# Performance work log

Hardware: AMD Instinct MI355X
Metric: run time of the kernel (lower is better)

## Reference

```python
import jax, jax.numpy as jnp
import numpy as np

B, S, D, H = 2, 2048, 1024, 16
DH = D // H
SCALE = 1.0 / float(np.sqrt(DH))


def setup_inputs() -> dict:
    key = jax.random.key(0)
    ks = jax.random.split(key, 9)
    std = 1.0 / float(np.sqrt(D))
    x = jax.random.normal(ks[0], (B, S, D), dtype=jnp.float32)
    # causal mask: True = masked (future positions)
    mask = jnp.triu(jnp.ones((S, S), dtype=bool), k=1)
    Wq = jax.random.normal(ks[1], (D, D), dtype=jnp.float32) * std
    Wk = jax.random.normal(ks[2], (D, D), dtype=jnp.float32) * std
    Wv = jax.random.normal(ks[3], (D, D), dtype=jnp.float32) * std
    Wo = jax.random.normal(ks[4], (D, D), dtype=jnp.float32) * std
    bq = jax.random.normal(ks[5], (D,), dtype=jnp.float32) * 0.01
    bk = jax.random.normal(ks[6], (D,), dtype=jnp.float32) * 0.01
    bv = jax.random.normal(ks[7], (D,), dtype=jnp.float32) * 0.01
    bo = jax.random.normal(ks[8], (D,), dtype=jnp.float32) * 0.01
    return {"x": x, "mask": mask, "Wq": Wq, "bq": bq, "Wk": Wk, "bk": bk,
            "Wv": Wv, "bv": bv, "Wo": Wo, "bo": bo}


def _split_heads(t):
    # (B, S, D) -> (B, H, S, DH)
    return t.reshape(B, S, H, DH).transpose(0, 2, 1, 3)


def reference(x, mask, Wq, bq, Wk, bk, Wv, bv, Wo, bo):
    # torch nn.Linear: y = x @ W.T + b
    q = _split_heads(x @ Wq.T + bq)
    k = _split_heads(x @ Wk.T + bk)
    v = _split_heads(x @ Wv.T + bv)
    # scores: (B, H, S, S)
    scores = jnp.einsum('bhsd,bhtd->bhst', q, k) * SCALE
    scores = jnp.where(mask[None, None, :, :], jnp.float32(-1e9), scores)
    attn = jax.nn.softmax(scores, axis=-1)
    attn = jnp.nan_to_num(attn, nan=0.0)
    out = jnp.einsum('bhst,bhtd->bhsd', attn, v)
    out = out.transpose(0, 2, 1, 3).reshape(B, S, D)
    return out @ Wo.T + bo
```

## Files before the change

### kernel.cpp

```cpp
#include <hip/hip_runtime.h>

#define S_LEN  2048
#define DMODEL 1024
#define NHEAD  16
#define DHEAD  64
#define SCALE_F 0.125f
#define SL2E_F 0.180336880f

typedef unsigned short ushort_t;
typedef __attribute__((ext_vector_type(8))) short bf16x8;
typedef __attribute__((ext_vector_type(4))) float f32x4;

typedef __attribute__((address_space(1))) void gv_t;
typedef __attribute__((address_space(3))) void lv_t;

__device__ __forceinline__ ushort_t f2bf(float f) {
    unsigned u = __builtin_bit_cast(unsigned, f);
    unsigned r = (u + 0x7FFFu + ((u >> 16) & 1u)) >> 16;
    return (ushort_t)r;
}

__device__ __forceinline__ unsigned cvtpk_bf16(float a, float b) {
    unsigned r;
    asm("v_cvt_pk_bf16_f32 %0, %1, %2" : "=v"(r) : "v"(a), "v"(b));
    return r;
}

__device__ __forceinline__ void gload16(const ushort_t* g, ushort_t* l) {
    __builtin_amdgcn_global_load_lds((gv_t*)g, (lv_t*)l, 16, 0, 0);
}

template<int N> __device__ __forceinline__ void wait_vmcnt() {
    if constexpr (N == 8)      asm volatile("s_waitcnt vmcnt(8)" ::: "memory");
    else if constexpr (N == 6) asm volatile("s_waitcnt vmcnt(6)" ::: "memory");
    else if constexpr (N == 4) asm volatile("s_waitcnt vmcnt(4)" ::: "memory");
    else if constexpr (N == 3) asm volatile("s_waitcnt vmcnt(3)" ::: "memory");
    else                       asm volatile("s_waitcnt vmcnt(0)" ::: "memory");
}

__global__ void cast_all(const float* __restrict__ x,
                         const float* __restrict__ Wq, const float* __restrict__ Wk,
                         const float* __restrict__ Wv, const float* __restrict__ Wo,
                         ushort_t* __restrict__ dst, int n4) {
    int i = blockIdx.x * blockDim.x + threadIdx.x;
    int stride = gridDim.x * blockDim.x;
    for (int idx = i; idx < n4; idx += stride) {
        const float* src; int off;
        if (idx < 1048576)      { src = x;  off = idx; }
        else if (idx < 1310720) { src = Wq; off = idx - 1048576; }
        else if (idx < 1572864) { src = Wk; off = idx - 1310720; }
        else if (idx < 1835008) { src = Wv; off = idx - 1572864; }
        else                    { src = Wo; off = idx - 1835008; }
        float4 f = ((const float4*)src)[off];
        ushort4 o;
        o.x = f2bf(f.x); o.y = f2bf(f.y); o.z = f2bf(f.z); o.w = f2bf(f.w);
        ((ushort4*)dst)[idx] = o;
    }
}

template<int MODE, int BM>
__launch_bounds__(256)
__global__ void gemm_bt(const ushort_t* __restrict__ A, const ushort_t* __restrict__ Bw,
                        const float* __restrict__ b0, const float* __restrict__ b1,
                        const float* __restrict__ b2,
                        void* __restrict__ out0, void* __restrict__ out1, void* __restrict__ out2,
                        int M, int N, int K) {
    constexpr int MF = BM / 32;
    constexpr int NLOADS = BM / 64 + 2;
    __shared__ ushort_t As[2][BM][32];
    __shared__ ushort_t Bs[2][128][32];
    const int tid  = threadIdx.x;
    const int lane = tid & 63;
    const int w    = tid >> 6;
    const int wr   = w >> 1, wc = w & 1;
    const int m0   = blockIdx.x * BM;
    const int n0   = blockIdx.y * 128;
    const int l15  = lane & 15;
    const int lg   = lane >> 4;
    const int srow = lane >> 2;
    const int scol = ((lane & 3) ^ ((lane >> 3) & 3)) * 8;
    const int ck   = (l15 >> 1) & 3;

    f32x4 acc[MF][4] = {};

    auto stage = [&](int buf, int k0) {
#pragma unroll
        for (int j = 0; j < BM / 64; j++) {
            const int rg = (w * (BM / 64) + j) * 16;
            gload16(A + (size_t)(m0 + rg + srow) * K + k0 + scol, &As[buf][rg][0]);
        }
#pragma unroll
        for (int j = 0; j < 2; j++) {
            const int rg = (w * 2 + j) * 16;
            gload16(Bw + (size_t)(n0 + rg + srow) * K + k0 + scol, &Bs[buf][rg][0]);
        }
    };

    stage(0, 0);
    int buf = 0;

    for (int k0 = 0; k0 < K; k0 += 32) {
        if (k0 + 32 < K) {
            stage(buf ^ 1, k0 + 32);
            wait_vmcnt<NLOADS>();
        } else {
            wait_vmcnt<0>();
        }
        __builtin_amdgcn_s_barrier();
        __builtin_amdgcn_sched_barrier(0);

        bf16x8 af[MF], bfr[4];
#pragma unroll
        for (int i = 0; i < MF; i++)
            af[i]  = *(const bf16x8*)&As[buf][wr*(BM/2) + i*16 + l15][(lg ^ ck) * 8];
#pragma unroll
        for (int i = 0; i < 4;  i++)
            bfr[i] = *(const bf16x8*)&Bs[buf][wc*64 + i*16 + l15][(lg ^ ck) * 8];

        __builtin_amdgcn_s_setprio(1);
#pragma unroll
        for (int mf = 0; mf < MF; mf++)
#pragma unroll
            for (int nf = 0; nf < 4; nf++)
                acc[mf][nf] = __builtin_amdgcn_mfma_f32_16x16x32_bf16(af[mf], bfr[nf], acc[mf][nf], 0, 0, 0);
        __builtin_amdgcn_s_setprio(0);

        asm volatile("s_waitcnt lgkmcnt(0)" ::: "memory");
        __builtin_amdgcn_sched_barrier(0);
        __builtin_amdgcn_s_barrier();
        buf ^= 1;
    }

#pragma unroll
    for (int mf = 0; mf < MF; mf++) {
#pragma unroll
        for (int nf = 0; nf < 4; nf++) {
            const int col = n0 + wc*64 + nf*16 + l15;
            if constexpr (MODE == 2) {
                const float bv = b0[col];
#pragma unroll
                for (int r = 0; r < 4; r++) {
                    const int row = m0 + wr*(BM/2) + mf*16 + lg*4 + r;
                    ((float*)out0)[(size_t)row * N + col] = acc[mf][nf][r] + bv;
                }
            } else {
                const int mat = col >> 10;
                const int c   = col & 1023;
                const int h   = c >> 6, dh = c & 63;
                const float* bp = (mat == 0) ? b0 : ((mat == 1) ? b1 : b2);
                const float bv = bp[c];
#pragma unroll
                for (int r = 0; r < 4; r++) {
                    const int row = m0 + wr*(BM/2) + mf*16 + lg*4 + r;
                    const int b = row >> 11, s = row & 2047;
                    float v = acc[mf][nf][r] + bv;
                    if (mat == 0) {
                        v *= SL2E_F;
                        ((ushort_t*)out0)[((size_t)(b*NHEAD + h) * S_LEN + s) * DHEAD + dh] = f2bf(v);
                    } else if (mat == 1)
                        ((ushort_t*)out1)[((size_t)(b*NHEAD + h) * S_LEN + s) * DHEAD + dh] = f2bf(v);
                    else
                        ((ushort_t*)out2)[((size_t)(b*NHEAD + h) * DHEAD + dh) * S_LEN + s] = f2bf(v);
                }
            }
        }
    }
}

__launch_bounds__(256, 4)
__global__ void attn_fwd(const ushort_t* __restrict__ Q, const ushort_t* __restrict__ Kh,
                         const ushort_t* __restrict__ Vt, ushort_t* __restrict__ Aout) {
    __shared__ ushort_t Ks[2][64][64];
    __shared__ ushort_t Vs[2][64][64];
    __shared__ ushort_t Ps[4][16][64];
    const int tid  = threadIdx.x;
    const int lane = tid & 63;
    const int w    = tid >> 6;
    const int l15  = lane & 15, lg = lane >> 4;
    const int bh   = blockIdx.x;
    const int y    = blockIdx.y;
    const int kq   = y >> 3, g0 = y & 7;
    const int qt   = (kq == 0) ? 2*g0 : (kq == 1) ? (31 - 2*g0)
                   : (kq == 2) ? (2*g0 + 1) : (30 - 2*g0);

    const size_t qkbase = (size_t)bh * S_LEN * DHEAD;
    const size_t vtbase = (size_t)bh * DHEAD * S_LEN;

    const int rsub  = lane >> 3;
    const int csw   = ((lane & 7) ^ rsub) * 8;
    const int swz   = (l15 & 7) * 8;
    const int psxor = (l15 & 7) << 4;

    const int qw = qt * 64 + w * 16;

    bf16x8 aq[2];
#pragma unroll
    for (int kc = 0; kc < 2; kc++)
        aq[kc] = *(const bf16x8*)(Q + qkbase + (size_t)(qw + l15) * DHEAD + kc*32 + lg*8);

    float m = -3.0e38f, l = 0.0f;
    f32x4 o[4] = {};

    auto stage = [&](int buf, int t) {
        const int kv0 = t * 64;
        const ushort_t* kp = Kh + qkbase + (size_t)kv0 * DHEAD;
        const ushort_t* vp = Vt + vtbase + kv0;
#pragma unroll
        for (int j2 = 0; j2 < 2; j2++) {
            const int j  = w * 2 + j2;
            const int rg = j * 8 + rsub;
            gload16(kp + (size_t)rg * DHEAD + csw, &Ks[buf][j*8][0]);
            gload16(vp + (size_t)rg * S_LEN + csw, &Vs[buf][j*8][0]);
        }
    };

    ushort_t* psw = &Ps[w][0][0];
    char* psrow = (char*)(psw + l15 * 64);

    stage(0, 0);
    int buf = 0;

    for (int t = 0; t <= qt; t++) {
        if (t < qt) {
            stage(buf ^ 1, t + 1);
            wait_vmcnt<4>();
        } else {
            wait_vmcnt<0>();
        }
        __builtin_amdgcn_s_barrier();
        __builtin_amdgcn_sched_barrier(0);

        f32x4 sacc[4] = {};
        __builtin_amdgcn_s_setprio(1);
#pragma unroll
        for (int kc = 0; kc < 2; kc++)
#pragma unroll
            for (int nf = 0; nf < 4; nf++) {
                bf16x8 bk = *(const bf16x8*)&Ks[buf][nf*16 + l15][(kc*32 + lg*8) ^ swz];
                sacc[nf] = __builtin_amdgcn_mfma_f32_16x16x32_bf16(bk, aq[kc], sacc[nf], 0, 0, 0);
            }
        __builtin_amdgcn_s_setprio(0);

        if (t == qt) {
            const int rowq = qw + l15;
            const int kv0  = t * 64;
#pragma unroll
            for (int nf = 0; nf < 4; nf++)
#pragma unroll
                for (int r = 0; r < 4; r++) {
                    const int colk = kv0 + nf*16 + lg*4 + r;
                    if (colk > rowq) sacc[nf][r] = -3.0e38f;
                }
        }

        float mnf[4];
#pragma unroll
        for (int nf = 0; nf < 4; nf++)
            mnf[nf] = fmaxf(fmaxf(sacc[nf][0], sacc[nf][1]), fmaxf(sacc[nf][2], sacc[nf][3]));
        float mx = fmaxf(fmaxf(mnf[0], mnf[1]), fmaxf(mnf[2], mnf[3]));
        mx = fmaxf(mx, __shfl_xor(mx, 16));
        mx = fmaxf(mx, __shfl_xor(mx, 32));

        const bool skip = __all(mx <= m + 8.0f);
        const float mn = skip ? m : fmaxf(m, mx);

        float snf[4];
#pragma unroll
        for (int nf = 0; nf < 4; nf++) {
            const float p0 = exp2f(sacc[nf][0] - mn);
            const float p1 = exp2f(sacc[nf][1] - mn);
            const float p2 = exp2f(sacc[nf][2] - mn);
            const float p3 = exp2f(sacc[nf][3] - mn);
            uint2 pk;
            pk.x = cvtpk_bf16(p0, p1);
            pk.y = cvtpk_bf16(p2, p3);
            *(uint2*)(psrow + (((nf*16 + lg*4) * 2) ^ psxor)) = pk;
            snf[nf] = (p0 + p1) + (p2 + p3);
        }
        float s = (snf[0] + snf[1]) + (snf[2] + snf[3]);
        s += __shfl_xor(s, 16);
        s += __shfl_xor(s, 32);

        if (skip) {
            l += s;
        } else {
            const float corr = exp2f(m - mn);
            m = mn;
            l = l * corr + s;
            float cf[4];
#pragma unroll
            for (int r = 0; r < 4; r++) cf[r] = __shfl(corr, lg*4 + r);
#pragma unroll
            for (int nf = 0; nf < 4; nf++)
#pragma unroll
                for (int r = 0; r < 4; r++) o[nf][r] *= cf[r];
        }

        __builtin_amdgcn_s_setprio(1);
#pragma unroll
        for (int kc = 0; kc < 2; kc++) {
            bf16x8 pa = *(const bf16x8*)(psrow + (((kc*32 + lg*8) * 2) ^ psxor));
#pragma unroll
            for (int nf = 0; nf < 4; nf++) {
                bf16x8 bv = *(const bf16x8*)&Vs[buf][nf*16 + l15][(kc*32 + lg*8) ^ swz];
                o[nf] = __builtin_amdgcn_mfma_f32_16x16x32_bf16(pa, bv, o[nf], 0, 0, 0);
            }
        }
        __builtin_amdgcn_s_setprio(0);

        asm volatile("s_waitcnt lgkmcnt(0)" ::: "memory");
        __builtin_amdgcn_sched_barrier(0);
        __builtin_amdgcn_s_barrier();
        buf ^= 1;
    }

    const int b = bh >> 4, h = bh & 15;
    const float inv = 1.0f / l;
#pragma unroll
    for (int r = 0; r < 4; r++) {
        const float ia = __shfl(inv, lg*4 + r);
        const int rowq = qw + lg*4 + r;
#pragma unroll
        for (int nf = 0; nf < 4; nf++)
            Aout[((size_t)(b * S_LEN) + rowq) * DMODEL + h*DHEAD + nf*16 + l15] = f2bf(o[nf][r] * ia);
    }
}

extern "C" void kernel_launch(void* const* d_in, const int* in_sizes, int n_in,
                              void* d_out, int out_size, void* d_ws, size_t ws_size,
                              hipStream_t stream) {
    (void)in_sizes; (void)n_in; (void)out_size; (void)ws_size;
    const float* x  = (const float*)d_in[0];
    const float* Wq = (const float*)d_in[2];
    const float* bq = (const float*)d_in[3];
    const float* Wk = (const float*)d_in[4];
    const float* bk = (const float*)d_in[5];
    const float* Wv = (const float*)d_in[6];
    const float* bv = (const float*)d_in[7];
    const float* Wo = (const float*)d_in[8];
    const float* bo = (const float*)d_in[9];

    char* ws = (char*)d_ws;
    ushort_t* xb    = (ushort_t*)(ws);
    ushort_t* Wqkvb = (ushort_t*)(ws + (8u  << 20));
    ushort_t* Wob   = (ushort_t*)(ws + (14u << 20));
    ushort_t* Qh    = (ushort_t*)(ws + (16u << 20));
    ushort_t* Kh    = (ushort_t*)(ws + (24u << 20));
    ushort_t* Vth   = (ushort_t*)(ws + (32u << 20));
    ushort_t* Ao    = (ushort_t*)(ws + (40u << 20));

    cast_all<<<2048, 256, 0, stream>>>(x, Wq, Wk, Wv, Wo, xb, 2097152);

    gemm_bt<0, 128><<<dim3(32, 24), 256, 0, stream>>>(xb, Wqkvb, bq, bk, bv,
                                                      Qh, Kh, Vth, 2*S_LEN, 3*DMODEL, DMODEL);

    attn_fwd<<<dim3(2*NHEAD, 32), 256, 0, stream>>>(Qh, Kh, Vth, Ao);

    gemm_bt<2, 64><<<dim3(64, 8), 256, 0, stream>>>(Ao, Wob, bo, nullptr, nullptr,
                                                    d_out, nullptr, nullptr, 2*S_LEN, DMODEL, DMODEL);
}
```

Before: 115.5 us.

## Triple-buffer GEMM LDS staging, remap workgroups by XCD, drop trailing barriers

The GEMM kernel moves from double to triple-buffered LDS, prefetching two K-tiles ahead so each iteration needs one barrier instead of two. Workgroup IDs are remapped so consecutive tiles land on the same XCD (8-way interleave), which is meant to improve L2 reuse. The attention kernel now issues its next-tile prefetch after the barrier, waits for all loads, and drops the trailing barrier. The costs are more LDS per block, possibly lower occupancy, and in attention a full vmcnt wait that exposes load latency.

```diff
diff --git a/kernel.cpp b/kernel.cpp
--- a/kernel.cpp
+++ b/kernel.cpp
@@ -67,14 +67,21 @@
                         int M, int N, int K) {
     constexpr int MF = BM / 32;
     constexpr int NLOADS = BM / 64 + 2;
-    __shared__ ushort_t As[2][BM][32];
-    __shared__ ushort_t Bs[2][128][32];
+    __shared__ ushort_t As[3][BM][32];
+    __shared__ ushort_t Bs[3][128][32];
     const int tid  = threadIdx.x;
     const int lane = tid & 63;
     const int w    = tid >> 6;
     const int wr   = w >> 1, wc = w & 1;
-    const int m0   = blockIdx.x * BM;
-    const int n0   = blockIdx.y * 128;
+
+    const int gx  = gridDim.x;
+    const int nwg = gx * gridDim.y;
+    const int wg  = blockIdx.y * gx + blockIdx.x;
+    const int q8  = nwg >> 3;
+    const int nid = (wg & 7) * q8 + (wg >> 3);
+    const int m0  = (nid % gx) * BM;
+    const int n0  = (nid / gx) * 128;
+
     const int l15  = lane & 15;
     const int lg   = lane >> 4;
     const int srow = lane >> 2;
@@ -83,39 +90,41 @@
 
     f32x4 acc[MF][4] = {};
 
-    auto stage = [&](int buf, int k0) {
+    auto stage = [&](int sbuf, int k0) {
 #pragma unroll
         for (int j = 0; j < BM / 64; j++) {
             const int rg = (w * (BM / 64) + j) * 16;
-            gload16(A + (size_t)(m0 + rg + srow) * K + k0 + scol, &As[buf][rg][0]);
+            gload16(A + (size_t)(m0 + rg + srow) * K + k0 + scol, &As[sbuf][rg][0]);
         }
 #pragma unroll
         for (int j = 0; j < 2; j++) {
             const int rg = (w * 2 + j) * 16;
-            gload16(Bw + (size_t)(n0 + rg + srow) * K + k0 + scol, &Bs[buf][rg][0]);
+            gload16(Bw + (size_t)(n0 + rg + srow) * K + k0 + scol, &Bs[sbuf][rg][0]);
         }
     };
 
+    const int nt = K >> 5;
     stage(0, 0);
-    int buf = 0;
-
-    for (int k0 = 0; k0 < K; k0 += 32) {
-        if (k0 + 32 < K) {
-            stage(buf ^ 1, k0 + 32);
-            wait_vmcnt<NLOADS>();
-        } else {
-            wait_vmcnt<0>();
-        }
+    stage(1, 32);
+    int bcur = 0;
+
+    for (int t = 0; t < nt; ++t) {
+        if (t + 1 < nt) wait_vmcnt<NLOADS>();
+        else           wait_vmcnt<0>();
         __builtin_amdgcn_s_barrier();
         __builtin_amdgcn_sched_barrier(0);
+        if (t + 2 < nt) {
+            int bst = bcur + 2; if (bst >= 3) bst -= 3;
+            stage(bst, (t + 2) << 5);
+        }
 
         bf16x8 af[MF], bfr[4];
 #pragma unroll
         for (int i = 0; i < MF; i++)
-            af[i]  = *(const bf16x8*)&As[buf][wr*(BM/2) + i*16 + l15][(lg ^ ck) * 8];
+            af[i]  = *(const bf16x8*)&As[bcur][wr*(BM/2) + i*16 + l15][(lg ^ ck) * 8];
 #pragma unroll
         for (int i = 0; i < 4;  i++)
-            bfr[i] = *(const bf16x8*)&Bs[buf][wc*64 + i*16 + l15][(lg ^ ck) * 8];
+            bfr[i] = *(const bf16x8*)&Bs[bcur][wc*64 + i*16 + l15][(lg ^ ck) * 8];
 
         __builtin_amdgcn_s_setprio(1);
 #pragma unroll
@@ -127,8 +136,7 @@
 
         asm volatile("s_waitcnt lgkmcnt(0)" ::: "memory");
         __builtin_amdgcn_sched_barrier(0);
-        __builtin_amdgcn_s_barrier();
-        buf ^= 1;
+        bcur = (bcur == 2) ? 0 : bcur + 1;
     }
 
 #pragma unroll
@@ -221,14 +229,10 @@
     int buf = 0;
 
     for (int t = 0; t <= qt; t++) {
-        if (t < qt) {
-            stage(buf ^ 1, t + 1);
-            wait_vmcnt<4>();
-        } else {
-            wait_vmcnt<0>();
-        }
+        wait_vmcnt<0>();
         __builtin_amdgcn_s_barrier();
         __builtin_amdgcn_sched_barrier(0);
+        if (t < qt) stage(buf ^ 1, t + 1);
 
         f32x4 sacc[4] = {};
         __builtin_amdgcn_s_setprio(1);
@@ -310,7 +314,6 @@
 
         asm volatile("s_waitcnt lgkmcnt(0)" ::: "memory");
         __builtin_amdgcn_sched_barrier(0);
-        __builtin_amdgcn_s_barrier();
         buf ^= 1;
     }
 
```

Measured after the change: 128.3 us. 11.1% more time.
